# Kernel optimization log

Measured on AMD Instinct MI355X. Metric: run time of the kernel, lower is better.

## Reference

```python
import jax, jax.numpy as jnp
import numpy as np

N_NODES = 50000
N_EDGES = 800000
IN_CH = 256
HID = 64
HEADS = 4
OUT_CH = 4
NEG_SLOPE = 0.2


def _add_self_loops(edge_index, n):
    ar = jnp.arange(n, dtype=edge_index.dtype)
    loops = jnp.stack([ar, ar])
    return jnp.concatenate([edge_index, loops], axis=1)


def _gat_conv(x, edge_index, W, att_src, att_dst, bias, heads, ch):
    # PyG GATConv (no edge features, add_self_loops=True, concat=True)
    n = x.shape[0]
    ei = _add_self_loops(edge_index, n)
    src, dst = ei[0], ei[1]
    xp = (x @ W).reshape(n, heads, ch)            # [N,H,C]
    a_src = (xp * att_src).sum(-1)                 # [N,H]
    a_dst = (xp * att_dst).sum(-1)                 # [N,H]
    alpha = jax.nn.leaky_relu(a_src[src] + a_dst[dst], NEG_SLOPE)  # [E',H]
    amax = jax.ops.segment_max(alpha, dst, num_segments=n)
    alpha = jnp.exp(alpha - amax[dst])
    denom = jax.ops.segment_sum(alpha, dst, num_segments=n)
    alpha = alpha / (denom[dst] + 1e-16)
    msg = xp[src] * alpha[:, :, None]              # [E',H,C]
    out = jax.ops.segment_sum(msg, dst, num_segments=n)  # [N,H,C]
    return out.reshape(n, heads * ch) + bias


def setup_inputs() -> dict:
    key = jax.random.key(0)
    ks = jax.random.split(key, 12)
    x = jax.random.normal(ks[0], (N_NODES, IN_CH), dtype=jnp.float32)
    edge_index = jax.random.randint(ks[1], (2, N_EDGES), 0, N_NODES, dtype=jnp.int64)
    w = jax.random.uniform(ks[2], (N_EDGES,), dtype=jnp.float32)
    s1 = 1.0 / np.sqrt(IN_CH)
    s2 = 1.0 / np.sqrt(HEADS * HID)
    return {
        "x": x, "edge_index": edge_index, "w": w,
        "W1": jax.random.normal(ks[3], (IN_CH, HEADS * HID), dtype=jnp.float32) * s1,
        "att_src1": jax.random.normal(ks[4], (1, HEADS, HID), dtype=jnp.float32) * s2,
        "att_dst1": jax.random.normal(ks[5], (1, HEADS, HID), dtype=jnp.float32) * s2,
        "b1": jnp.zeros((HEADS * HID,), dtype=jnp.float32),
        "W2": jax.random.normal(ks[6], (HEADS * HID, HID), dtype=jnp.float32) * s2,
        "att_src2": jax.random.normal(ks[7], (1, 1, HID), dtype=jnp.float32) * s2,
        "att_dst2": jax.random.normal(ks[8], (1, 1, HID), dtype=jnp.float32) * s2,
        "b2": jnp.zeros((HID,), dtype=jnp.float32),
        "Wc": jax.random.normal(ks[9], (2 * HID, OUT_CH), dtype=jnp.float32) * (1.0 / np.sqrt(2 * HID)),
        "bc": jnp.zeros((OUT_CH,), dtype=jnp.float32),
    }


def reference(x, edge_index, w, W1, att_src1, att_dst1, b1,
              W2, att_src2, att_dst2, b2, Wc, bc):
    # w (edge_attr) is ignored: GATConv was built without edge_dim, so no lin_edge.
    h = _gat_conv(x, edge_index, W1, att_src1, att_dst1, b1, HEADS, HID)
    h = jax.nn.relu(h)
    h = _gat_conv(h, edge_index, W2, att_src2, att_dst2, b2, 1, HID)
    row, col = edge_index[0], edge_index[1]
    edge_emb = jnp.concatenate([h[row], h[col]], axis=-1)  # [E, 2*HID]
    return edge_emb @ Wc + bc
```

## Files before the change

### kernel.cpp

```cpp
#include <hip/hip_runtime.h>


#define NEG 0.2f

typedef __attribute__((ext_vector_type(8))) short bf16x8;
typedef __attribute__((ext_vector_type(4))) float f32x4;

__device__ __forceinline__ unsigned short f2bf(float f) {
    unsigned int u = __float_as_uint(f);
    unsigned int r = (u + 0x7FFFu + ((u >> 16) & 1u)) >> 16;
    return (unsigned short)r;
}
__device__ __forceinline__ float bf2f(unsigned short h) {
    return __uint_as_float(((unsigned int)h) << 16);
}
__device__ __forceinline__ float bflo(unsigned int u) { return __uint_as_float(u << 16); }
__device__ __forceinline__ float bfhi(unsigned int u) { return __uint_as_float(u & 0xFFFF0000u); }
__device__ __forceinline__ float lrelu(float x) { return x > 0.f ? x : NEG * x; }

__device__ __forceinline__ void async16(const void* g, void* l) {
    __builtin_amdgcn_global_load_lds(
        (const __attribute__((address_space(1))) unsigned int*)g,
        (__attribute__((address_space(3))) unsigned int*)l, 16, 0, 0);
}


__global__ __launch_bounds__(256) void k_init(int* deg, int* cur, int n) {
    int i = blockIdx.x * 256 + threadIdx.x;
    if (i < n) { deg[i] = 1; cur[i] = 0; }
}

__global__ __launch_bounds__(256) void k_hist(const int* __restrict__ ei, int* deg, int E) {
    int e = blockIdx.x * 256 + threadIdx.x;
    if (e < E) atomicAdd(&deg[ei[E + e]], 1);
}

__global__ __launch_bounds__(256) void k_bsum(const int* __restrict__ deg, int* __restrict__ bsum, int n) {
    int i = blockIdx.x * 256 + threadIdx.x;
    int v = (i < n) ? deg[i] : 0;
#pragma unroll
    for (int off = 1; off < 64; off <<= 1) v += __shfl_xor(v, off, 64);
    __shared__ int ws[4];
    int wv = threadIdx.x >> 6, l = threadIdx.x & 63;
    if (l == 0) ws[wv] = v;
    __syncthreads();
    if (threadIdx.x == 0) bsum[blockIdx.x] = ws[0] + ws[1] + ws[2] + ws[3];
}

__global__ __launch_bounds__(256) void k_bscan(const int* __restrict__ bsum, int* __restrict__ boff,
                                               int* __restrict__ rowptr, int nb, int n) {
    __shared__ int s[256];
    int t = threadIdx.x;
    int v = (t < nb) ? bsum[t] : 0;
    s[t] = v;
    __syncthreads();
    for (int off = 1; off < 256; off <<= 1) {
        int u = (t >= off) ? s[t - off] : 0;
        __syncthreads();
        s[t] += u;
        __syncthreads();
    }
    if (t < nb) boff[t] = s[t] - v;
    if (t == nb - 1) rowptr[n] = s[t];
}

__global__ __launch_bounds__(256) void k_rowptr(const int* __restrict__ deg, const int* __restrict__ boff,
                                                int* __restrict__ rowptr, int n) {
    __shared__ int s[256];
    int i = blockIdx.x * 256 + threadIdx.x;
    int t = threadIdx.x;
    int v = (i < n) ? deg[i] : 0;
    s[t] = v;
    __syncthreads();
    for (int off = 1; off < 256; off <<= 1) {
        int u = (t >= off) ? s[t - off] : 0;
        __syncthreads();
        s[t] += u;
        __syncthreads();
    }
    if (i < n) rowptr[i] = boff[blockIdx.x] + s[t] - v;
}

__global__ __launch_bounds__(256) void k_scatter(const int* __restrict__ ei, const int* __restrict__ rowptr,
                                                 int* cur, int* csr_src, int E, int N) {
    int e = blockIdx.x * 256 + threadIdx.x;
    if (e < E) {
        int d = ei[E + e];
        int pos = rowptr[d] + atomicAdd(&cur[d], 1);
        csr_src[pos] = ei[e];
    } else if (e < E + N) {
        int i = e - E;
        int pos = rowptr[i] + atomicAdd(&cur[i], 1);
        csr_src[pos] = i;
    }
}


__global__ __launch_bounds__(256) void k_pack_hi(const float* __restrict__ src,
                                                 unsigned short* __restrict__ hi, long n4) {
    long i = (long)blockIdx.x * 256 + threadIdx.x;
    long stride = (long)gridDim.x * 256;
    for (; i < n4; i += stride) {
        float4 v = ((const float4*)src)[i];
        ((ushort4*)hi)[i] = make_ushort4(f2bf(v.x), f2bf(v.y), f2bf(v.z), f2bf(v.w));
    }
}

__global__ __launch_bounds__(256) void k_pack_wT(const float* __restrict__ W,
                                                 unsigned short* __restrict__ hiT,
                                                 unsigned short* __restrict__ loT, int K, int N) {
    int t = blockIdx.x * 256 + threadIdx.x;
    if (t >= K * N) return;
    int n = t / K, k = t - n * K;
    float v = W[(size_t)k * N + n];
    unsigned short h = f2bf(v);
    hiT[t] = h;
    loT[t] = f2bf(v - bf2f(h));
}

template<int WGM, int WGN>
__global__ __launch_bounds__(256, 2) void k_gemm_lds(const unsigned short* __restrict__ Ah,
                                                     const unsigned short* __restrict__ BhT,
                                                     const unsigned short* __restrict__ BlT,
                                                     unsigned short* __restrict__ Cb, int M, int N, int K,
                                                     const float* __restrict__ att_s,
                                                     const float* __restrict__ att_d,
                                                     float* __restrict__ as, float* __restrict__ ad, int H) {
    constexpr int BM = WGM * 64, BN = WGN * 64;
    __shared__ char lds[BM * 128 + BN * 256];
    char* LAh = lds;
    char* LBh = lds + BM * 128;
    char* LBl = lds + BM * 128 + BN * 128;

    const int t = threadIdx.x, wv = t >> 6, l = t & 63;
    const int r = l & 15, hk = l >> 4;
    const int m0 = blockIdx.x * BM;
    const int n0 = blockIdx.y * BN;
    const int wr = wv / WGN, wc = wv % WGN;
    const int wrow0 = wr * 64, wcol0 = wc * 64;

    f32x4 acc[4][4];
#pragma unroll
    for (int i = 0; i < 4; i++)
#pragma unroll
        for (int j = 0; j < 4; j++) acc[i][j] = f32x4{0, 0, 0, 0};

    const int lrow8 = l >> 3;
    const int cbs = ((l & 7) ^ lrow8) << 4;
    const size_t K2 = (size_t)K * 2;
    const int NCH = K >> 6;

    for (int c = 0; c < NCH; ++c) {
        const int kk2 = c * 128;
        {
            const int SA = BM / 8;
            for (int i = wv; i < SA; i += 4) {
                int row = i * 8 + lrow8;
                size_t go = (size_t)(m0 + row) * K2 + kk2 + cbs;
                async16((const char*)Ah + go, LAh + i * 1024);
            }
            const int SB = BN / 8;
            for (int i = wv; i < SB; i += 4) {
                int row = i * 8 + lrow8;
                size_t go = (size_t)(n0 + row) * K2 + kk2 + cbs;
                async16((const char*)BhT + go, LBh + i * 1024);
                async16((const char*)BlT + go, LBl + i * 1024);
            }
        }
        __syncthreads();
#pragma unroll
        for (int ks = 0; ks < 2; ++ks) {
            const int cb = ks * 64 + hk * 16;
            bf16x8 a_h[4], b_h[4], b_l[4];
#pragma unroll
            for (int fm = 0; fm < 4; ++fm) {
                int row = wrow0 + fm * 16 + r;
                int ad_ = row * 128 + (cb ^ ((row & 7) << 4));
                a_h[fm] = *(const bf16x8*)(LAh + ad_);
            }
#pragma unroll
            for (int fn = 0; fn < 4; ++fn) {
                int row = wcol0 + fn * 16 + r;
                int ad_ = row * 128 + (cb ^ ((row & 7) << 4));
                b_h[fn] = *(const bf16x8*)(LBh + ad_);
                b_l[fn] = *(const bf16x8*)(LBl + ad_);
            }
#pragma unroll
            for (int fm = 0; fm < 4; ++fm)
#pragma unroll
                for (int fn = 0; fn < 4; ++fn) {
                    acc[fm][fn] = __builtin_amdgcn_mfma_f32_16x16x32_bf16(a_h[fm], b_h[fn], acc[fm][fn], 0, 0, 0);
                    acc[fm][fn] = __builtin_amdgcn_mfma_f32_16x16x32_bf16(a_h[fm], b_l[fn], acc[fm][fn], 0, 0, 0);
                }
        }
        if (c + 1 < NCH) __syncthreads();
    }

#pragma unroll
    for (int fm = 0; fm < 4; ++fm)
#pragma unroll
        for (int fn = 0; fn < 4; ++fn)
#pragma unroll
            for (int j = 0; j < 4; ++j) {
                int m = m0 + wrow0 + fm * 16 + hk * 4 + j;
                if (m < M) Cb[(size_t)m * N + n0 + wcol0 + fn * 16 + r] = f2bf(acc[fm][fn][j]);
            }

    {
        int head = (n0 + wcol0) >> 6;
        float satt[4], datt[4];
#pragma unroll
        for (int fn = 0; fn < 4; ++fn) {
            satt[fn] = att_s[head * 64 + fn * 16 + r];
            datt[fn] = att_d[head * 64 + fn * 16 + r];
        }
#pragma unroll
        for (int fm = 0; fm < 4; ++fm)
#pragma unroll
            for (int j = 0; j < 4; ++j) {
                float ps = 0.f, pd = 0.f;
#pragma unroll
                for (int fn = 0; fn < 4; ++fn) {
                    ps += satt[fn] * acc[fm][fn][j];
                    pd += datt[fn] * acc[fm][fn][j];
                }
#pragma unroll
                for (int off = 1; off <= 8; off <<= 1) {
                    ps += __shfl_xor(ps, off, 64);
                    pd += __shfl_xor(pd, off, 64);
                }
                if (r == 0) {
                    int m = m0 + wrow0 + fm * 16 + hk * 4 + j;
                    if (m < M) { as[m * H + head] = ps; ad[m * H + head] = pd; }
                }
            }
    }
}


__global__ __launch_bounds__(256) void k_gather1(const unsigned short* __restrict__ xpb,
                                                 const float* __restrict__ as, const float* __restrict__ ad,
                                                 const int* __restrict__ rowptr, const int* __restrict__ csr_src,
                                                 const float* __restrict__ b1,
                                                 unsigned short* __restrict__ h1h, int M) {
    int wv = threadIdx.x >> 6, lane = threadIdx.x & 63;
    int n = blockIdx.x * 4 + wv;
    if (n >= M) return;
    int h = lane >> 4;
    float adv = ad[n * 4 + h];
    int start = rowptr[n], end = rowptr[n + 1];
    float a0[4] = {0.f, 0.f, 0.f, 0.f}, a1[4] = {0.f, 0.f, 0.f, 0.f};
    float den0 = 0.f, den1 = 0.f;
    int e = start;
    for (; e + 3 < end; e += 4) {
        int s0 = csr_src[e], s1 = csr_src[e + 1], s2 = csr_src[e + 2], s3 = csr_src[e + 3];
        uint2 v0 = *(const uint2*)(xpb + (size_t)s0 * 256 + lane * 4);
        uint2 v1 = *(const uint2*)(xpb + (size_t)s1 * 256 + lane * 4);
        uint2 v2 = *(const uint2*)(xpb + (size_t)s2 * 256 + lane * 4);
        uint2 v3 = *(const uint2*)(xpb + (size_t)s3 * 256 + lane * 4);
        float w0 = as[s0 * 4 + h], w1 = as[s1 * 4 + h], w2 = as[s2 * 4 + h], w3 = as[s3 * 4 + h];
        float p0 = __expf(lrelu(w0 + adv));
        float p1 = __expf(lrelu(w1 + adv));
        float p2 = __expf(lrelu(w2 + adv));
        float p3 = __expf(lrelu(w3 + adv));
        den0 += p0 + p2; den1 += p1 + p3;
        a0[0] += p0 * bflo(v0.x); a0[1] += p0 * bfhi(v0.x);
        a0[2] += p0 * bflo(v0.y); a0[3] += p0 * bfhi(v0.y);
        a1[0] += p1 * bflo(v1.x); a1[1] += p1 * bfhi(v1.x);
        a1[2] += p1 * bflo(v1.y); a1[3] += p1 * bfhi(v1.y);
        a0[0] += p2 * bflo(v2.x); a0[1] += p2 * bfhi(v2.x);
        a0[2] += p2 * bflo(v2.y); a0[3] += p2 * bfhi(v2.y);
        a1[0] += p3 * bflo(v3.x); a1[1] += p3 * bfhi(v3.x);
        a1[2] += p3 * bflo(v3.y); a1[3] += p3 * bfhi(v3.y);
    }
    for (; e < end; ++e) {
        int s0 = csr_src[e];
        uint2 v0 = *(const uint2*)(xpb + (size_t)s0 * 256 + lane * 4);
        float p0 = __expf(lrelu(as[s0 * 4 + h] + adv));
        den0 += p0;
        a0[0] += p0 * bflo(v0.x); a0[1] += p0 * bfhi(v0.x);
        a0[2] += p0 * bflo(v0.y); a0[3] += p0 * bfhi(v0.y);
    }
    float dinv = 1.f / (den0 + den1 + 1e-16f);
    const float4 bb = *(const float4*)(b1 + lane * 4);
    float o0 = fmaxf((a0[0] + a1[0]) * dinv + bb.x, 0.f);
    float o1 = fmaxf((a0[1] + a1[1]) * dinv + bb.y, 0.f);
    float o2 = fmaxf((a0[2] + a1[2]) * dinv + bb.z, 0.f);
    float o3 = fmaxf((a0[3] + a1[3]) * dinv + bb.w, 0.f);
    uint2 H;
    H.x = (unsigned)f2bf(o0) | ((unsigned)f2bf(o1) << 16);
    H.y = (unsigned)f2bf(o2) | ((unsigned)f2bf(o3) << 16);
    *(uint2*)(h1h + (size_t)n * 256 + lane * 4) = H;
}

__global__ __launch_bounds__(256) void k_gather2(const unsigned short* __restrict__ xp2b,
                                                 const float* __restrict__ as, const float* __restrict__ ad,
                                                 const int* __restrict__ rowptr, const int* __restrict__ csr_src,
                                                 const float* __restrict__ b2, const float* __restrict__ Wc,
                                                 float* __restrict__ uv, int M) {
    int wv = threadIdx.x >> 6, lane = threadIdx.x & 63;
    int n = blockIdx.x * 4 + wv;
    if (n >= M) return;
    int g = lane >> 4, q = lane & 15;
    float adv = ad[n];
    int start = rowptr[n], end = rowptr[n + 1];
    float acc[4] = {0.f, 0.f, 0.f, 0.f};
    float den = 0.f;
    for (int e = start; e < end; e += 4) {
        int ee = e + g;
        bool ok = ee < end;
        int s = csr_src[ok ? ee : start];
        uint2 v = *(const uint2*)(xp2b + (size_t)s * 64 + q * 4);
        float pw = ok ? __expf(lrelu(as[s] + adv)) : 0.f;
        den += pw;
        acc[0] += pw * bflo(v.x); acc[1] += pw * bfhi(v.x);
        acc[2] += pw * bflo(v.y); acc[3] += pw * bfhi(v.y);
    }
#pragma unroll
    for (int j = 0; j < 4; j++) {
        acc[j] += __shfl_xor(acc[j], 16, 64);
        acc[j] += __shfl_xor(acc[j], 32, 64);
    }
    den += __shfl_xor(den, 16, 64);
    den += __shfl_xor(den, 32, 64);
    float dinv = 1.f / (den + 1e-16f);
    float pr[8] = {0.f, 0.f, 0.f, 0.f, 0.f, 0.f, 0.f, 0.f};
#pragma unroll
    for (int j = 0; j < 4; j++) {
        int c = q * 4 + j;
        float val = acc[j] * dinv + b2[c];
#pragma unroll
        for (int k = 0; k < 4; k++) {
            pr[k]     += val * Wc[c * 4 + k];
            pr[4 + k] += val * Wc[(64 + c) * 4 + k];
        }
    }
#pragma unroll
    for (int off = 1; off <= 8; off <<= 1)
#pragma unroll
        for (int j = 0; j < 8; j++) pr[j] += __shfl_xor(pr[j], off, 64);
    if (lane == 0) {
        float4* o = (float4*)(uv + (size_t)n * 8);
        o[0] = make_float4(pr[0], pr[1], pr[2], pr[3]);
        o[1] = make_float4(pr[4], pr[5], pr[6], pr[7]);
    }
}

__global__ __launch_bounds__(256) void k_classify(const int* __restrict__ ei, const float* __restrict__ uv,
                                                  const float* __restrict__ bc, float* __restrict__ out, int E) {
    int e = blockIdx.x * 256 + threadIdx.x;
    if (e >= E) return;
    int r = ei[e];
    int c = ei[E + e];
    float4 u = *(const float4*)(uv + (size_t)r * 8);
    float4 v = *(const float4*)(uv + (size_t)c * 8 + 4);
    float4 o;
    o.x = u.x + v.x + bc[0];
    o.y = u.y + v.y + bc[1];
    o.z = u.z + v.z + bc[2];
    o.w = u.w + v.w + bc[3];
    *(float4*)(out + (size_t)e * 4) = o;
}


extern "C" void kernel_launch(void* const* d_in, const int* in_sizes, int n_in,
                              void* d_out, int out_size, void* d_ws, size_t ws_size,
                              hipStream_t stream) {
    const float* x    = (const float*)d_in[0];
    const int*   ei   = (const int*)d_in[1];
    const float* W1   = (const float*)d_in[3];
    const float* atS1 = (const float*)d_in[4];
    const float* atD1 = (const float*)d_in[5];
    const float* b1   = (const float*)d_in[6];
    const float* W2   = (const float*)d_in[7];
    const float* atS2 = (const float*)d_in[8];
    const float* atD2 = (const float*)d_in[9];
    const float* b2   = (const float*)d_in[10];
    const float* Wc   = (const float*)d_in[11];
    const float* bc   = (const float*)d_in[12];
    float* out = (float*)d_out;

    const int Nn = in_sizes[0] / 256;
    const int E = in_sizes[1] / 2;
    const int Etot = E + Nn;
    const int NB = (Nn + 255) / 256;

    char* w = (char*)d_ws;
    size_t off = 0;
    auto alloc = [&](size_t b) { size_t o = off; off = (o + b + 255) & ~(size_t)255; return o; };
    size_t oXH  = alloc((size_t)Nn * 256 * 2);
    size_t oXPB = alloc((size_t)Nn * 256 * 2);
    size_t oAS1 = alloc((size_t)Nn * 4 * 4);
    size_t oAD1 = alloc((size_t)Nn * 4 * 4);
    size_t oDEG = alloc((size_t)Nn * 4);
    size_t oCUR = alloc((size_t)Nn * 4);
    size_t oRP  = alloc((size_t)(Nn + 1) * 4);
    size_t oCSR = alloc((size_t)Etot * 4);
    size_t oW1H = alloc((size_t)256 * 256 * 2);
    size_t oW1L = alloc((size_t)256 * 256 * 2);
    size_t oW2H = alloc((size_t)256 * 64 * 2);
    size_t oW2L = alloc((size_t)256 * 64 * 2);
    size_t oBS  = alloc((size_t)NB * 4);
    size_t oBO  = alloc((size_t)NB * 4);
    (void)ws_size;

    unsigned short* xh   = (unsigned short*)(w + oXH);
    unsigned short* h1h  = (unsigned short*)(w + oXH);
    unsigned short* xpb  = (unsigned short*)(w + oXPB);
    unsigned short* xp2b = (unsigned short*)(w + oXPB);
    float* uv  = (float*)(w + oXPB + (size_t)Nn * 64 * 2 + 256);
    uv = (float*)(((uintptr_t)uv + 255) & ~(uintptr_t)255);
    float* as1 = (float*)(w + oAS1);
    float* ad1 = (float*)(w + oAD1);
    float* as2 = (float*)(w + oAS1);
    float* ad2 = (float*)(w + oAD1);
    int* deg    = (int*)(w + oDEG);
    int* cur    = (int*)(w + oCUR);
    int* rowptr = (int*)(w + oRP);
    int* csr    = (int*)(w + oCSR);
    int* bsum   = (int*)(w + oBS);
    int* boff   = (int*)(w + oBO);
    unsigned short* W1hT = (unsigned short*)(w + oW1H);
    unsigned short* W1lT = (unsigned short*)(w + oW1L);
    unsigned short* W2hT = (unsigned short*)(w + oW2H);
    unsigned short* W2lT = (unsigned short*)(w + oW2L);

    k_init<<<NB, 256, 0, stream>>>(deg, cur, Nn);
    k_hist<<<(E + 255) / 256, 256, 0, stream>>>(ei, deg, E);
    k_bsum<<<NB, 256, 0, stream>>>(deg, bsum, Nn);
    k_bscan<<<1, 256, 0, stream>>>(bsum, boff, rowptr, NB, Nn);
    k_rowptr<<<NB, 256, 0, stream>>>(deg, boff, rowptr, Nn);
    k_scatter<<<(Etot + 255) / 256, 256, 0, stream>>>(ei, rowptr, cur, csr, E, Nn);

    k_pack_hi<<<2048, 256, 0, stream>>>(x, xh, (long)Nn * 64);
    k_pack_wT<<<(256 * 256 + 255) / 256, 256, 0, stream>>>(W1, W1hT, W1lT, 256, 256);
    k_pack_wT<<<(256 * 64 + 255) / 256, 256, 0, stream>>>(W2, W2hT, W2lT, 256, 64);

    {
        dim3 g((Nn + 127) / 128, 2);
        k_gemm_lds<2, 2><<<g, 256, 0, stream>>>(xh, W1hT, W1lT, xpb, Nn, 256, 256,
                                                atS1, atD1, as1, ad1, 4);
    }
    k_gather1<<<(Nn + 3) / 4, 256, 0, stream>>>(xpb, as1, ad1, rowptr, csr, b1, h1h, Nn);

    {
        dim3 g((Nn + 255) / 256, 1);
        k_gemm_lds<4, 1><<<g, 256, 0, stream>>>(h1h, W2hT, W2lT, xp2b, Nn, 64, 256,
                                                atS2, atD2, as2, ad2, 1);
    }
    k_gather2<<<(Nn + 3) / 4, 256, 0, stream>>>(xp2b, as2, ad2, rowptr, csr, b2, Wc, uv, Nn);

    k_classify<<<(E + 255) / 256, 256, 0, stream>>>(ei, uv, bc, out, E);
}
```

Baseline: 285.7 us.

## Widen gather loads to 16 bytes and split edges across half-waves

In layer 1, each half of the wavefront now loads a whole 256-element bf16 row with 16-byte loads and takes alternate edges, so two edges are fetched per wave step. The two halves are combined with one cross-lane shuffle at the end. Layer 2 handles 8 edges per step with 16-byte loads, which needs one extra shuffle stage. The two weight-packing kernels are merged into a single launch to save one launch. Each lane now holds more accumulator registers, and layer 1 needs extra tail handling for odd edge counts.

```diff
diff --git a/kernel.cpp b/kernel.cpp
--- a/kernel.cpp
+++ b/kernel.cpp
@@ -106,16 +106,29 @@
     }
 }
 
-__global__ __launch_bounds__(256) void k_pack_wT(const float* __restrict__ W,
-                                                 unsigned short* __restrict__ hiT,
-                                                 unsigned short* __restrict__ loT, int K, int N) {
+__global__ __launch_bounds__(256) void k_pack_w2(const float* __restrict__ W1,
+                                                 const float* __restrict__ W2,
+                                                 unsigned short* __restrict__ W1hT,
+                                                 unsigned short* __restrict__ W1lT,
+                                                 unsigned short* __restrict__ W2hT,
+                                                 unsigned short* __restrict__ W2lT) {
     int t = blockIdx.x * 256 + threadIdx.x;
-    if (t >= K * N) return;
-    int n = t / K, k = t - n * K;
-    float v = W[(size_t)k * N + n];
-    unsigned short h = f2bf(v);
-    hiT[t] = h;
-    loT[t] = f2bf(v - bf2f(h));
+    if (t < 256 * 256) {
+        int n = t >> 8, k = t & 255;
+        float v = W1[k * 256 + n];
+        unsigned short h = f2bf(v);
+        W1hT[t] = h;
+        W1lT[t] = f2bf(v - bf2f(h));
+    } else {
+        int t2 = t - 256 * 256;
+        if (t2 < 64 * 256) {
+            int n = t2 >> 8, k = t2 & 255;
+            float v = W2[k * 64 + n];
+            unsigned short h = f2bf(v);
+            W2hT[t2] = h;
+            W2lT[t2] = f2bf(v - bf2f(h));
+        }
+    }
 }
 
 template<int WGM, int WGN>
@@ -246,51 +259,78 @@
     int wv = threadIdx.x >> 6, lane = threadIdx.x & 63;
     int n = blockIdx.x * 4 + wv;
     if (n >= M) return;
-    int h = lane >> 4;
+    int half = lane >> 5;
+    int q = lane & 31;
+    int h = q >> 3;
     float adv = ad[n * 4 + h];
     int start = rowptr[n], end = rowptr[n + 1];
-    float a0[4] = {0.f, 0.f, 0.f, 0.f}, a1[4] = {0.f, 0.f, 0.f, 0.f};
-    float den0 = 0.f, den1 = 0.f;
+    float acc[8] = {0.f, 0.f, 0.f, 0.f, 0.f, 0.f, 0.f, 0.f};
+    float den = 0.f;
+
+    auto edge = [&](int s, uint4 v) {
+        float p = __expf(lrelu(as[s * 4 + h] + adv));
+        den += p;
+        acc[0] += p * bflo(v.x); acc[1] += p * bfhi(v.x);
+        acc[2] += p * bflo(v.y); acc[3] += p * bfhi(v.y);
+        acc[4] += p * bflo(v.z); acc[5] += p * bfhi(v.z);
+        acc[6] += p * bflo(v.w); acc[7] += p * bfhi(v.w);
+    };
+
     int e = start;
-    for (; e + 3 < end; e += 4) {
-        int s0 = csr_src[e], s1 = csr_src[e + 1], s2 = csr_src[e + 2], s3 = csr_src[e + 3];
-        uint2 v0 = *(const uint2*)(xpb + (size_t)s0 * 256 + lane * 4);
-        uint2 v1 = *(const uint2*)(xpb + (size_t)s1 * 256 + lane * 4);
-        uint2 v2 = *(const uint2*)(xpb + (size_t)s2 * 256 + lane * 4);
-        uint2 v3 = *(const uint2*)(xpb + (size_t)s3 * 256 + lane * 4);
-        float w0 = as[s0 * 4 + h], w1 = as[s1 * 4 + h], w2 = as[s2 * 4 + h], w3 = as[s3 * 4 + h];
-        float p0 = __expf(lrelu(w0 + adv));
-        float p1 = __expf(lrelu(w1 + adv));
-        float p2 = __expf(lrelu(w2 + adv));
-        float p3 = __expf(lrelu(w3 + adv));
-        den0 += p0 + p2; den1 += p1 + p3;
-        a0[0] += p0 * bflo(v0.x); a0[1] += p0 * bfhi(v0.x);
-        a0[2] += p0 * bflo(v0.y); a0[3] += p0 * bfhi(v0.y);
-        a1[0] += p1 * bflo(v1.x); a1[1] += p1 * bfhi(v1.x);
-        a1[2] += p1 * bflo(v1.y); a1[3] += p1 * bfhi(v1.y);
-        a0[0] += p2 * bflo(v2.x); a0[1] += p2 * bfhi(v2.x);
-        a0[2] += p2 * bflo(v2.y); a0[3] += p2 * bfhi(v2.y);
-        a1[0] += p3 * bflo(v3.x); a1[1] += p3 * bfhi(v3.x);
-        a1[2] += p3 * bflo(v3.y); a1[3] += p3 * bfhi(v3.y);
-    }
-    for (; e < end; ++e) {
-        int s0 = csr_src[e];
-        uint2 v0 = *(const uint2*)(xpb + (size_t)s0 * 256 + lane * 4);
-        float p0 = __expf(lrelu(as[s0 * 4 + h] + adv));
-        den0 += p0;
-        a0[0] += p0 * bflo(v0.x); a0[1] += p0 * bfhi(v0.x);
-        a0[2] += p0 * bflo(v0.y); a0[3] += p0 * bfhi(v0.y);
-    }
-    float dinv = 1.f / (den0 + den1 + 1e-16f);
-    const float4 bb = *(const float4*)(b1 + lane * 4);
-    float o0 = fmaxf((a0[0] + a1[0]) * dinv + bb.x, 0.f);
-    float o1 = fmaxf((a0[1] + a1[1]) * dinv + bb.y, 0.f);
-    float o2 = fmaxf((a0[2] + a1[2]) * dinv + bb.z, 0.f);
-    float o3 = fmaxf((a0[3] + a1[3]) * dinv + bb.w, 0.f);
-    uint2 H;
-    H.x = (unsigned)f2bf(o0) | ((unsigned)f2bf(o1) << 16);
-    H.y = (unsigned)f2bf(o2) | ((unsigned)f2bf(o3) << 16);
-    *(uint2*)(h1h + (size_t)n * 256 + lane * 4) = H;
+    for (; e + 7 < end; e += 8) {
+        int sa = csr_src[e + half];
+        int sb = csr_src[e + 2 + half];
+        int sc = csr_src[e + 4 + half];
+        int sd = csr_src[e + 6 + half];
+        uint4 va = *(const uint4*)(xpb + (size_t)sa * 256 + q * 8);
+        uint4 vb = *(const uint4*)(xpb + (size_t)sb * 256 + q * 8);
+        uint4 vc = *(const uint4*)(xpb + (size_t)sc * 256 + q * 8);
+        uint4 vd = *(const uint4*)(xpb + (size_t)sd * 256 + q * 8);
+        edge(sa, va); edge(sb, vb); edge(sc, vc); edge(sd, vd);
+    }
+    if (e + 3 < end) {
+        int sa = csr_src[e + half];
+        int sb = csr_src[e + 2 + half];
+        uint4 va = *(const uint4*)(xpb + (size_t)sa * 256 + q * 8);
+        uint4 vb = *(const uint4*)(xpb + (size_t)sb * 256 + q * 8);
+        edge(sa, va); edge(sb, vb);
+        e += 4;
+    }
+    if (e + 1 < end) {
+        int sa = csr_src[e + half];
+        uint4 va = *(const uint4*)(xpb + (size_t)sa * 256 + q * 8);
+        edge(sa, va);
+        e += 2;
+    }
+    if (e < end && half == 0) {
+        int sa = csr_src[e];
+        uint4 va = *(const uint4*)(xpb + (size_t)sa * 256 + q * 8);
+        edge(sa, va);
+    }
+
+#pragma unroll
+    for (int j = 0; j < 8; j++) acc[j] += __shfl_xor(acc[j], 32, 64);
+    den += __shfl_xor(den, 32, 64);
+
+    float dinv = 1.f / (den + 1e-16f);
+    float4 b0 = *(const float4*)(b1 + q * 8);
+    float4 b4 = *(const float4*)(b1 + q * 8 + 4);
+    float o0 = fmaxf(acc[0] * dinv + b0.x, 0.f);
+    float o1 = fmaxf(acc[1] * dinv + b0.y, 0.f);
+    float o2 = fmaxf(acc[2] * dinv + b0.z, 0.f);
+    float o3 = fmaxf(acc[3] * dinv + b0.w, 0.f);
+    float o4 = fmaxf(acc[4] * dinv + b4.x, 0.f);
+    float o5 = fmaxf(acc[5] * dinv + b4.y, 0.f);
+    float o6 = fmaxf(acc[6] * dinv + b4.z, 0.f);
+    float o7 = fmaxf(acc[7] * dinv + b4.w, 0.f);
+    if (half == 0) {
+        uint4 Hv;
+        Hv.x = (unsigned)f2bf(o0) | ((unsigned)f2bf(o1) << 16);
+        Hv.y = (unsigned)f2bf(o2) | ((unsigned)f2bf(o3) << 16);
+        Hv.z = (unsigned)f2bf(o4) | ((unsigned)f2bf(o5) << 16);
+        Hv.w = (unsigned)f2bf(o6) | ((unsigned)f2bf(o7) << 16);
+        *(uint4*)(h1h + (size_t)n * 256 + q * 8) = Hv;
+    }
 }
 
 __global__ __launch_bounds__(256) void k_gather2(const unsigned short* __restrict__ xp2b,
@@ -301,33 +341,37 @@
     int wv = threadIdx.x >> 6, lane = threadIdx.x & 63;
     int n = blockIdx.x * 4 + wv;
     if (n >= M) return;
-    int g = lane >> 4, q = lane & 15;
+    int g = lane >> 3, q = lane & 7;
     float adv = ad[n];
     int start = rowptr[n], end = rowptr[n + 1];
-    float acc[4] = {0.f, 0.f, 0.f, 0.f};
+    float acc[8] = {0.f, 0.f, 0.f, 0.f, 0.f, 0.f, 0.f, 0.f};
     float den = 0.f;
-    for (int e = start; e < end; e += 4) {
+    for (int e = start; e < end; e += 8) {
         int ee = e + g;
         bool ok = ee < end;
         int s = csr_src[ok ? ee : start];
-        uint2 v = *(const uint2*)(xp2b + (size_t)s * 64 + q * 4);
+        uint4 v = *(const uint4*)(xp2b + (size_t)s * 64 + q * 8);
         float pw = ok ? __expf(lrelu(as[s] + adv)) : 0.f;
         den += pw;
         acc[0] += pw * bflo(v.x); acc[1] += pw * bfhi(v.x);
         acc[2] += pw * bflo(v.y); acc[3] += pw * bfhi(v.y);
-    }
-#pragma unroll
-    for (int j = 0; j < 4; j++) {
+        acc[4] += pw * bflo(v.z); acc[5] += pw * bfhi(v.z);
+        acc[6] += pw * bflo(v.w); acc[7] += pw * bfhi(v.w);
+    }
+#pragma unroll
+    for (int j = 0; j < 8; j++) {
+        acc[j] += __shfl_xor(acc[j], 8, 64);
         acc[j] += __shfl_xor(acc[j], 16, 64);
         acc[j] += __shfl_xor(acc[j], 32, 64);
     }
+    den += __shfl_xor(den, 8, 64);
     den += __shfl_xor(den, 16, 64);
     den += __shfl_xor(den, 32, 64);
     float dinv = 1.f / (den + 1e-16f);
     float pr[8] = {0.f, 0.f, 0.f, 0.f, 0.f, 0.f, 0.f, 0.f};
 #pragma unroll
-    for (int j = 0; j < 4; j++) {
-        int c = q * 4 + j;
+    for (int j = 0; j < 8; j++) {
+        int c = q * 8 + j;
         float val = acc[j] * dinv + b2[c];
 #pragma unroll
         for (int k = 0; k < 4; k++) {
@@ -336,7 +380,7 @@
         }
     }
 #pragma unroll
-    for (int off = 1; off <= 8; off <<= 1)
+    for (int off = 1; off <= 4; off <<= 1)
 #pragma unroll
         for (int j = 0; j < 8; j++) pr[j] += __shfl_xor(pr[j], off, 64);
     if (lane == 0) {
@@ -433,8 +477,7 @@
     k_scatter<<<(Etot + 255) / 256, 256, 0, stream>>>(ei, rowptr, cur, csr, E, Nn);
 
     k_pack_hi<<<2048, 256, 0, stream>>>(x, xh, (long)Nn * 64);
-    k_pack_wT<<<(256 * 256 + 255) / 256, 256, 0, stream>>>(W1, W1hT, W1lT, 256, 256);
-    k_pack_wT<<<(256 * 64 + 255) / 256, 256, 0, stream>>>(W2, W2hT, W2lT, 256, 64);
+    k_pack_w2<<<(256 * 256 + 64 * 256 + 255) / 256, 256, 0, stream>>>(W1, W2, W1hT, W1lT, W2hT, W2lT);
 
     {
         dim3 g((Nn + 127) / 128, 2);
```

Result: slower. 333.0 us (+16.5%).
